# Optimization experiments

Hardware: AMD Instinct MI355X
Metric: run time of the kernel (lower is better)

## Reference

```python
import jax, jax.numpy as jnp
import numpy as np
from jax import lax

NUM_SAMPLE = 1024   # init_kwargs: num_sample
RADIUS = 0.1        # init_kwargs: ball_query_radius (compared against SQUARED distance, as in original)


def setup_inputs() -> dict:
    key = jax.random.key(0)
    x = jax.random.normal(key, (4, 32768, 131), dtype=jnp.float32)  # [B, N, 3+C]
    return {"x": x}


def _fps_single(pts, num_sample):
    # pts: [N, 3]. Faithful to source: seed index is overwritten at i=0, so the
    # only effect of the seed is the first distance update; we use a
    # deterministic seed of 0 instead of python random.randint.
    n = pts.shape[0]

    def step(carry, _):
        closest, sel = carry
        d = jnp.sum((pts[sel] - pts) ** 2, axis=-1)      # [N]
        closest = jnp.minimum(d, closest)
        sel = jnp.argmax(closest).astype(jnp.int32)
        return (closest, sel), sel

    init = (jnp.full((n,), jnp.inf, dtype=jnp.float32), jnp.int32(0))
    _, idx = lax.scan(step, init, None, length=num_sample)
    return idx  # [M] int32


def _ball_query_counts(pts, idx, radius):
    # pts: [N,3], idx: [M]. Original builds variable-length index lists; the
    # jit-static equivalent is the membership mask d2 <= radius. We return the
    # per-centroid member counts (summary of the mask).
    cent = pts[idx]                                                 # [M, 3]
    d2 = jnp.sum((cent[:, None, :] - pts[None, :, :]) ** 2, axis=-1)  # [M, N]
    return jnp.sum(d2 <= radius, axis=-1).astype(jnp.int32)          # [M]


def reference(x):
    pts = x[:, :, :3]                                    # [B, N, 3]
    idx = jax.vmap(lambda p: _fps_single(p, NUM_SAMPLE))(pts)            # [B, M]
    counts = jax.vmap(lambda p, i: _ball_query_counts(p, i, RADIUS))(pts, idx)  # [B, M]
    # Original forward returns x unchanged; idx/counts are returned as well so
    # the FPS + ball-query compute is observable and not dead-code-eliminated.
    return (x, idx, counts)
```

## Files before the change

kernel.cpp:

```cpp
#include <hip/hip_runtime.h>
#include <math.h>

#define B 4
#define N 32768
#define D 131
#define S 1024
#define RAD2 0.1f
#define G 16
#define TPB 256
#define PPT (N / G / TPB)

__global__ void copy_x_kernel(const float* __restrict__ x, float* __restrict__ out) {
    const size_t total4 = (size_t)B * N * D / 4;
    const float4* __restrict__ src = (const float4*)x;
    float4* __restrict__ dst = (float4*)out;
    for (size_t i = (size_t)blockIdx.x * blockDim.x + threadIdx.x; i < total4;
         i += (size_t)gridDim.x * blockDim.x)
        dst[i] = src[i];
}

__global__ void pack_kernel(const float* __restrict__ x, float* __restrict__ ws) {
    int i = blockIdx.x * blockDim.x + threadIdx.x;
    if (i < B * N) {
        const float* __restrict__ s = x + (size_t)i * D;
        float a = s[0], bb = s[1], c = s[2];
        ws[i]             = a;
        ws[B * N + i]     = bb;
        ws[2 * B * N + i] = c;
        float4* w4 = (float4*)(ws + (size_t)3 * B * N);
        w4[i] = make_float4(a, bb, c, 0.0f);
    }
}

__launch_bounds__(TPB)
__global__ void fps_kernel(const float* __restrict__ ws,
                           unsigned long long* __restrict__ gslot,
                           float* __restrict__ out_idx,
                           int* __restrict__ idx_int) {
    const int b = blockIdx.x / G;
    const int g = blockIdx.x % G;
    const int t = threadIdx.x;
    const int w = t >> 6;
    const int lane = t & 63;

    __shared__ unsigned long long s_slot[2][4];
    __shared__ int s_selbuf[2];

    const float* __restrict__ px = ws + (size_t)b * N;
    const float* __restrict__ py = ws + (size_t)(B + b) * N;
    const float* __restrict__ pz = ws + (size_t)(2 * B + b) * N;
    const float4* __restrict__ p4 = (const float4*)(ws + (size_t)3 * B * N) + (size_t)b * N;
    unsigned long long* __restrict__ slots = gslot + (size_t)b * 2 * G;

    const int base = g * (N / G);
    float lx[PPT], ly[PPT], lz[PPT], lcl[PPT];
    #pragma unroll
    for (int i = 0; i < PPT / 2; ++i) {
        int p = base + 2 * t + 2 * TPB * i;
        float2 vx = *(const float2*)&px[p];
        float2 vy = *(const float2*)&py[p];
        float2 vz = *(const float2*)&pz[p];
        lx[2*i] = vx.x; lx[2*i+1] = vx.y;
        ly[2*i] = vy.x; ly[2*i+1] = vy.y;
        lz[2*i] = vz.x; lz[2*i+1] = vz.y;
        lcl[2*i] = INFINITY; lcl[2*i+1] = INFINITY;
    }

    float4 c4 = p4[0];

    for (int s = 0; s < S; ++s) {
        const float cx = c4.x, cy = c4.y, cz = c4.z;

        float best = -INFINITY;
        int   bidx = 0;
        #pragma unroll
        for (int i = 0; i < PPT / 2; ++i) {
            const int p = base + 2 * t + 2 * TPB * i;
            {
                float dx = __fsub_rn(cx, lx[2*i]);
                float dy = __fsub_rn(cy, ly[2*i]);
                float dz = __fsub_rn(cz, lz[2*i]);
                float d2 = __fadd_rn(__fadd_rn(__fmul_rn(dx, dx), __fmul_rn(dy, dy)),
                                     __fmul_rn(dz, dz));
                float c = fminf(lcl[2*i], d2);
                lcl[2*i] = c;
                if (c > best) { best = c; bidx = p; }
            }
            {
                float dx = __fsub_rn(cx, lx[2*i+1]);
                float dy = __fsub_rn(cy, ly[2*i+1]);
                float dz = __fsub_rn(cz, lz[2*i+1]);
                float d2 = __fadd_rn(__fadd_rn(__fmul_rn(dx, dx), __fmul_rn(dy, dy)),
                                     __fmul_rn(dz, dz));
                float c = fminf(lcl[2*i+1], d2);
                lcl[2*i+1] = c;
                if (c > best) { best = c; bidx = p + 1; }
            }
        }

        unsigned hi = __float_as_uint(best);
        unsigned lo2 = (unsigned)(32767 - bidx);

        #define FPS_COMBINE(OHI, OLO) \
            { unsigned _oh = (OHI), _ol = (OLO); \
              if (_oh > hi || (_oh == hi && _ol > lo2)) { hi = _oh; lo2 = _ol; } }
        { unsigned a = (unsigned)__builtin_amdgcn_update_dpp(0, (int)hi, 0xB1, 0xf, 0xf, true);
          unsigned c2 = (unsigned)__builtin_amdgcn_update_dpp(0, (int)lo2, 0xB1, 0xf, 0xf, true);
          FPS_COMBINE(a, c2); }
        { unsigned a = (unsigned)__builtin_amdgcn_update_dpp(0, (int)hi, 0x4E, 0xf, 0xf, true);
          unsigned c2 = (unsigned)__builtin_amdgcn_update_dpp(0, (int)lo2, 0x4E, 0xf, 0xf, true);
          FPS_COMBINE(a, c2); }
        { unsigned a = (unsigned)__builtin_amdgcn_update_dpp(0, (int)hi, 0x141, 0xf, 0xf, true);
          unsigned c2 = (unsigned)__builtin_amdgcn_update_dpp(0, (int)lo2, 0x141, 0xf, 0xf, true);
          FPS_COMBINE(a, c2); }
        { unsigned a = (unsigned)__builtin_amdgcn_update_dpp(0, (int)hi, 0x140, 0xf, 0xf, true);
          unsigned c2 = (unsigned)__builtin_amdgcn_update_dpp(0, (int)lo2, 0x140, 0xf, 0xf, true);
          FPS_COMBINE(a, c2); }
        { unsigned a = (unsigned)__builtin_amdgcn_ds_swizzle((int)hi, 0x401F);
          unsigned c2 = (unsigned)__builtin_amdgcn_ds_swizzle((int)lo2, 0x401F);
          FPS_COMBINE(a, c2); }
        { unsigned a = (unsigned)__shfl_xor((int)hi, 32, 64);
          unsigned c2 = (unsigned)__shfl_xor((int)lo2, 32, 64);
          FPS_COMBINE(a, c2); }
        #undef FPS_COMBINE

        const int buf = s & 1;
        const unsigned tag = (unsigned)(s + 1);
        if (lane == 0)
            s_slot[buf][w] = ((unsigned long long)hi << 32) | ((unsigned long long)lo2 << 17) | tag;
        __syncthreads();

        if (w == 0) {
            unsigned long long k = s_slot[buf][0];
            #pragma unroll
            for (int j = 1; j < 4; ++j) { unsigned long long v = s_slot[buf][j]; if (v > k) k = v; }
            if (lane == 0)
                __hip_atomic_store(&slots[buf * G + g], k, __ATOMIC_RELAXED,
                                   __HIP_MEMORY_SCOPE_AGENT);
            unsigned long long kk;
            unsigned long long* myslot = &slots[buf * G + (lane & 15)];
            do {
                kk = __hip_atomic_load(myslot, __ATOMIC_RELAXED, __HIP_MEMORY_SCOPE_AGENT);
            } while (__any((unsigned)(kk & 0x7FFull) != tag));
            #pragma unroll
            for (int off = 1; off < 16; off <<= 1) {
                unsigned long long o = (unsigned long long)__shfl_xor((long long)kk, off, 64);
                if (o > kk) kk = o;
            }
            if (lane == 0) {
                int sel = 32767 - (int)((kk >> 17) & 0x7FFF);
                s_selbuf[buf] = sel;
                if (g == 0) {
                    out_idx[b * S + s] = (float)sel;
                    idx_int[b * S + s] = sel;
                }
            }
        }
        __syncthreads();
        c4 = p4[s_selbuf[buf]];
    }
}

__launch_bounds__(256)
__global__ void ballq_kernel(const float* __restrict__ ws,
                             const int* __restrict__ idx_int,
                             float* __restrict__ out_counts) {
    __shared__ int s_part[4];
    const int b = blockIdx.x >> 10;
    const int j = blockIdx.x & 1023;
    const int t = threadIdx.x;
    const float* __restrict__ px = ws + (size_t)b * N;
    const float* __restrict__ py = ws + (size_t)(B + b) * N;
    const float* __restrict__ pz = ws + (size_t)(2 * B + b) * N;

    const int ci = idx_int[b * S + j];
    const float cx = px[ci], cy = py[ci], cz = pz[ci];

    int cnt = 0;
    #pragma unroll 4
    for (int p = t; p < N; p += 256) {
        float dx = __fsub_rn(cx, px[p]);
        float dy = __fsub_rn(cy, py[p]);
        float dz = __fsub_rn(cz, pz[p]);
        float d2 = __fadd_rn(__fadd_rn(__fmul_rn(dx, dx), __fmul_rn(dy, dy)),
                             __fmul_rn(dz, dz));
        cnt += (d2 <= RAD2) ? 1 : 0;
    }
    #pragma unroll
    for (int off = 1; off < 64; off <<= 1)
        cnt += __shfl_xor(cnt, off, 64);
    if ((t & 63) == 0) s_part[t >> 6] = cnt;
    __syncthreads();
    if (t == 0)
        out_counts[b * S + j] = (float)(s_part[0] + s_part[1] + s_part[2] + s_part[3]);
}

extern "C" void kernel_launch(void* const* d_in, const int* in_sizes, int n_in,
                              void* d_out, int out_size, void* d_ws, size_t ws_size,
                              hipStream_t stream) {
    const float* x = (const float*)d_in[0];
    float* out = (float*)d_out;
    float* ws = (float*)d_ws;
    int* idx_int = (int*)(ws + (size_t)7 * B * N);
    unsigned long long* gslot = (unsigned long long*)(idx_int + B * S);

    float* out_x      = out;
    float* out_idx    = out + (size_t)B * N * D;
    float* out_counts = out_idx + (size_t)B * S;

    hipMemsetAsync(gslot, 0, (size_t)B * 2 * G * sizeof(unsigned long long), stream);

    hipLaunchKernelGGL(pack_kernel, dim3((B * N + 255) / 256), dim3(256), 0, stream, x, ws);
    hipLaunchKernelGGL(copy_x_kernel, dim3(2048), dim3(256), 0, stream, x, out_x);
    hipLaunchKernelGGL(fps_kernel, dim3(B * G), dim3(TPB), 0, stream, ws, gslot, out_idx, idx_int);
    hipLaunchKernelGGL(ballq_kernel, dim3(B * S), dim3(256), 0, stream, ws, idx_int, out_counts);
}
```

Measured before the change: 2.001 ms.

## Replace block-level FPS reduction with flat per-wave global slot exchange

The FPS kernel now uses 8 blocks of 512 threads per batch. Every wave publishes its candidate directly to a global slot array of 64 entries per batch, and every wave polls all 64 slots and reduces them itself. This removes the two __syncthreads and the shared-memory stage from each of the 1024 serial iterations. In exchange every wave spins on global atomics each step, which adds L2 polling traffic, and an empty asm statement pins the point coordinates in registers.

```diff
diff --git a/kernel.cpp b/kernel.cpp
--- a/kernel.cpp
+++ b/kernel.cpp
@@ -6,9 +6,10 @@
 #define D 131
 #define S 1024
 #define RAD2 0.1f
-#define G 16
-#define TPB 256
-#define PPT (N / G / TPB)
+#define G 8
+#define TPB 512
+#define PPT 8
+#define WAVES_PER_BATCH 64
 
 __global__ void copy_x_kernel(const float* __restrict__ x, float* __restrict__ out) {
     const size_t total4 = (size_t)B * N * D / 4;
@@ -40,17 +41,14 @@
     const int b = blockIdx.x / G;
     const int g = blockIdx.x % G;
     const int t = threadIdx.x;
-    const int w = t >> 6;
     const int lane = t & 63;
-
-    __shared__ unsigned long long s_slot[2][4];
-    __shared__ int s_selbuf[2];
+    const int wave = (g * TPB + t) >> 6;
 
     const float* __restrict__ px = ws + (size_t)b * N;
     const float* __restrict__ py = ws + (size_t)(B + b) * N;
     const float* __restrict__ pz = ws + (size_t)(2 * B + b) * N;
     const float4* __restrict__ p4 = (const float4*)(ws + (size_t)3 * B * N) + (size_t)b * N;
-    unsigned long long* __restrict__ slots = gslot + (size_t)b * 2 * G;
+    unsigned long long* __restrict__ slots = gslot + (size_t)b * 2 * WAVES_PER_BATCH;
 
     const int base = g * (N / G);
     float lx[PPT], ly[PPT], lz[PPT], lcl[PPT];
@@ -64,6 +62,9 @@
         ly[2*i] = vy.x; ly[2*i+1] = vy.y;
         lz[2*i] = vz.x; lz[2*i+1] = vz.y;
         lcl[2*i] = INFINITY; lcl[2*i+1] = INFINITY;
+        asm volatile("" : "+v"(lx[2*i]), "+v"(lx[2*i+1]),
+                          "+v"(ly[2*i]), "+v"(ly[2*i+1]),
+                          "+v"(lz[2*i]), "+v"(lz[2*i+1]));
     }
 
     float4 c4 = p4[0];
@@ -126,38 +127,32 @@
 
         const int buf = s & 1;
         const unsigned tag = (unsigned)(s + 1);
-        if (lane == 0)
-            s_slot[buf][w] = ((unsigned long long)hi << 32) | ((unsigned long long)lo2 << 17) | tag;
-        __syncthreads();
-
-        if (w == 0) {
-            unsigned long long k = s_slot[buf][0];
-            #pragma unroll
-            for (int j = 1; j < 4; ++j) { unsigned long long v = s_slot[buf][j]; if (v > k) k = v; }
-            if (lane == 0)
-                __hip_atomic_store(&slots[buf * G + g], k, __ATOMIC_RELAXED,
-                                   __HIP_MEMORY_SCOPE_AGENT);
-            unsigned long long kk;
-            unsigned long long* myslot = &slots[buf * G + (lane & 15)];
-            do {
-                kk = __hip_atomic_load(myslot, __ATOMIC_RELAXED, __HIP_MEMORY_SCOPE_AGENT);
-            } while (__any((unsigned)(kk & 0x7FFull) != tag));
-            #pragma unroll
-            for (int off = 1; off < 16; off <<= 1) {
-                unsigned long long o = (unsigned long long)__shfl_xor((long long)kk, off, 64);
-                if (o > kk) kk = o;
-            }
-            if (lane == 0) {
-                int sel = 32767 - (int)((kk >> 17) & 0x7FFF);
-                s_selbuf[buf] = sel;
-                if (g == 0) {
-                    out_idx[b * S + s] = (float)sel;
-                    idx_int[b * S + s] = sel;
-                }
-            }
-        }
-        __syncthreads();
-        c4 = p4[s_selbuf[buf]];
+        if (lane == 0) {
+            unsigned long long k = ((unsigned long long)hi << 32) |
+                                   ((unsigned long long)lo2 << 17) | tag;
+            __hip_atomic_store(&slots[buf * WAVES_PER_BATCH + wave], k,
+                               __ATOMIC_RELAXED, __HIP_MEMORY_SCOPE_AGENT);
+        }
+
+        unsigned long long kk;
+        unsigned long long* myslot = &slots[buf * WAVES_PER_BATCH + lane];
+        do {
+            kk = __hip_atomic_load(myslot, __ATOMIC_RELAXED, __HIP_MEMORY_SCOPE_AGENT);
+        } while (__any((unsigned)(kk & 0x7FFull) != tag));
+
+        #pragma unroll
+        for (int off = 1; off < 64; off <<= 1) {
+            unsigned long long o = (unsigned long long)__shfl_xor((long long)kk, off, 64);
+            if (o > kk) kk = o;
+        }
+        int sel = 32767 - (int)((kk >> 17) & 0x7FFF);
+        sel = __builtin_amdgcn_readfirstlane(sel);
+
+        if (g == 0 && t == 0) {
+            out_idx[b * S + s] = (float)sel;
+            idx_int[b * S + s] = sel;
+        }
+        c4 = p4[sel];
     }
 }
 
@@ -208,7 +203,8 @@
     float* out_idx    = out + (size_t)B * N * D;
     float* out_counts = out_idx + (size_t)B * S;
 
-    hipMemsetAsync(gslot, 0, (size_t)B * 2 * G * sizeof(unsigned long long), stream);
+    hipMemsetAsync(gslot, 0, (size_t)B * 2 * WAVES_PER_BATCH * sizeof(unsigned long long),
+                   stream);
 
     hipLaunchKernelGGL(pack_kernel, dim3((B * N + 255) / 256), dim3(256), 0, stream, x, ws);
     hipLaunchKernelGGL(copy_x_kernel, dim3(2048), dim3(256), 0, stream, x, out_x);
```

New measurement: 4.344 ms. +117.1%, slower.

## Fuse x copy into FPS kernel and remove second per-step barrier

Applied to the files above, without the earlier changes.

The bulk copy of x into the output now runs in extra blocks of the FPS launch (192 copy blocks next to 64 FPS blocks), so the copy overlaps the latency-bound FPS loop instead of running as a separate kernel. Inside FPS, every wave now reads the per-wave keys, polls the global slots itself and broadcasts the selected index with readfirstlane. This removes the second __syncthreads and the shared-memory broadcast on each of the 1024 steps. The risks are that the copy traffic contends with the FPS polling and loads, and that all four waves now spin on global atomics.

```diff
diff --git a/kernel.cpp b/kernel.cpp
--- a/kernel.cpp
+++ b/kernel.cpp
@@ -8,16 +8,9 @@
 #define RAD2 0.1f
 #define G 16
 #define TPB 256
-#define PPT (N / G / TPB)
-
-__global__ void copy_x_kernel(const float* __restrict__ x, float* __restrict__ out) {
-    const size_t total4 = (size_t)B * N * D / 4;
-    const float4* __restrict__ src = (const float4*)x;
-    float4* __restrict__ dst = (float4*)out;
-    for (size_t i = (size_t)blockIdx.x * blockDim.x + threadIdx.x; i < total4;
-         i += (size_t)gridDim.x * blockDim.x)
-        dst[i] = src[i];
-}
+#define PPT 8
+#define NFPS (B * G)
+#define COPY_BLOCKS 192
 
 __global__ void pack_kernel(const float* __restrict__ x, float* __restrict__ ws) {
     int i = blockIdx.x * blockDim.x + threadIdx.x;
@@ -33,18 +26,29 @@
 }
 
 __launch_bounds__(TPB)
-__global__ void fps_kernel(const float* __restrict__ ws,
-                           unsigned long long* __restrict__ gslot,
-                           float* __restrict__ out_idx,
-                           int* __restrict__ idx_int) {
-    const int b = blockIdx.x / G;
-    const int g = blockIdx.x % G;
+__global__ void fps_copy_kernel(const float* __restrict__ x,
+                                const float* __restrict__ ws,
+                                unsigned long long* __restrict__ gslot,
+                                float* __restrict__ out_idx,
+                                int* __restrict__ idx_int,
+                                float* __restrict__ out_x) {
+    if (blockIdx.x >= NFPS) {
+        const size_t total4 = (size_t)B * N * D / 4;
+        const float4* __restrict__ src = (const float4*)x;
+        float4* __restrict__ dst = (float4*)out_x;
+        for (size_t i = (size_t)(blockIdx.x - NFPS) * TPB + threadIdx.x; i < total4;
+             i += (size_t)COPY_BLOCKS * TPB)
+            dst[i] = src[i];
+        return;
+    }
+
+    const int b = blockIdx.x >> 4;
+    const int g = blockIdx.x & 15;
     const int t = threadIdx.x;
+    const int lane = t & 63;
     const int w = t >> 6;
-    const int lane = t & 63;
-
-    __shared__ unsigned long long s_slot[2][4];
-    __shared__ int s_selbuf[2];
+
+    __shared__ unsigned long long s_wk[2][4];
 
     const float* __restrict__ px = ws + (size_t)b * N;
     const float* __restrict__ py = ws + (size_t)(B + b) * N;
@@ -98,7 +102,7 @@
             }
         }
 
-        unsigned hi = __float_as_uint(best);
+        unsigned hi  = __float_as_uint(best);
         unsigned lo2 = (unsigned)(32767 - bidx);
 
         #define FPS_COMBINE(OHI, OLO) \
@@ -126,38 +130,37 @@
 
         const int buf = s & 1;
         const unsigned tag = (unsigned)(s + 1);
-        if (lane == 0)
-            s_slot[buf][w] = ((unsigned long long)hi << 32) | ((unsigned long long)lo2 << 17) | tag;
+        const unsigned long long mykey = ((unsigned long long)hi << 32) |
+                                         ((unsigned long long)lo2 << 17) | tag;
+        if (lane == 0) s_wk[buf][w] = mykey;
         __syncthreads();
 
-        if (w == 0) {
-            unsigned long long k = s_slot[buf][0];
-            #pragma unroll
-            for (int j = 1; j < 4; ++j) { unsigned long long v = s_slot[buf][j]; if (v > k) k = v; }
-            if (lane == 0)
-                __hip_atomic_store(&slots[buf * G + g], k, __ATOMIC_RELAXED,
-                                   __HIP_MEMORY_SCOPE_AGENT);
-            unsigned long long kk;
-            unsigned long long* myslot = &slots[buf * G + (lane & 15)];
-            do {
-                kk = __hip_atomic_load(myslot, __ATOMIC_RELAXED, __HIP_MEMORY_SCOPE_AGENT);
-            } while (__any((unsigned)(kk & 0x7FFull) != tag));
-            #pragma unroll
-            for (int off = 1; off < 16; off <<= 1) {
-                unsigned long long o = (unsigned long long)__shfl_xor((long long)kk, off, 64);
-                if (o > kk) kk = o;
-            }
-            if (lane == 0) {
-                int sel = 32767 - (int)((kk >> 17) & 0x7FFF);
-                s_selbuf[buf] = sel;
-                if (g == 0) {
-                    out_idx[b * S + s] = (float)sel;
-                    idx_int[b * S + s] = sel;
-                }
-            }
+        unsigned long long bk = s_wk[buf][0];
+        #pragma unroll
+        for (int j = 1; j < 4; ++j) { unsigned long long v = s_wk[buf][j]; if (v > bk) bk = v; }
+        if (t == 0)
+            __hip_atomic_store(&slots[buf * G + g], bk, __ATOMIC_RELAXED,
+                               __HIP_MEMORY_SCOPE_AGENT);
+
+        unsigned long long kk;
+        unsigned long long* myslot = &slots[buf * G + (lane & 15)];
+        do {
+            kk = __hip_atomic_load(myslot, __ATOMIC_RELAXED, __HIP_MEMORY_SCOPE_AGENT);
+        } while (__any((unsigned)(kk & 0x7FFull) != tag));
+
+        #pragma unroll
+        for (int off = 1; off < 16; off <<= 1) {
+            unsigned long long o = (unsigned long long)__shfl_xor((long long)kk, off, 64);
+            if (o > kk) kk = o;
         }
-        __syncthreads();
-        c4 = p4[s_selbuf[buf]];
+        int sel = 32767 - (int)((kk >> 17) & 0x7FFF);
+        sel = __builtin_amdgcn_readfirstlane(sel);
+
+        if (g == 0 && t == 0) {
+            out_idx[(size_t)b * S + s] = (float)sel;
+            idx_int[b * S + s] = sel;
+        }
+        c4 = p4[sel];
     }
 }
 
@@ -211,7 +214,7 @@
     hipMemsetAsync(gslot, 0, (size_t)B * 2 * G * sizeof(unsigned long long), stream);
 
     hipLaunchKernelGGL(pack_kernel, dim3((B * N + 255) / 256), dim3(256), 0, stream, x, ws);
-    hipLaunchKernelGGL(copy_x_kernel, dim3(2048), dim3(256), 0, stream, x, out_x);
-    hipLaunchKernelGGL(fps_kernel, dim3(B * G), dim3(TPB), 0, stream, ws, gslot, out_idx, idx_int);
+    hipLaunchKernelGGL(fps_copy_kernel, dim3(NFPS + COPY_BLOCKS), dim3(TPB), 0, stream,
+                       x, ws, gslot, out_idx, idx_int, out_x);
     hipLaunchKernelGGL(ballq_kernel, dim3(B * S), dim3(256), 0, stream, ws, idx_int, out_counts);
 }
```

Result: slower. 2.353 ms (+17.6%).
